# Kernel tuning notes

Measured on AMD Instinct MI355X. Metric: run time of the kernel, lower is better.

The kernel has to match this reference:

```python
import jax, jax.numpy as jnp
import numpy as np

N = 50000      # nodes
E = 600000     # edges
DIN = 128      # dim_in
DOUT = 128     # dim_out (mulhead=1)
DG = 64        # dim_gate


def setup_inputs() -> dict:
    key = jax.random.key(0)
    ks = jax.random.split(key, 10)
    rows = jax.random.randint(ks[0], (E,), 0, N, dtype=jnp.int32)   # dest nodes
    cols = jax.random.randint(ks[1], (E,), 0, N, dtype=jnp.int32)   # src nodes
    vals = jax.random.uniform(ks[2], (E,), dtype=jnp.float32)       # adj_norm values
    feat = jax.random.normal(ks[3], (N, DIN), dtype=jnp.float32)
    s = 1.0 / np.sqrt(DIN)
    W0 = jax.random.normal(ks[4], (DIN, DOUT), dtype=jnp.float32) * s
    b0 = jnp.zeros((DOUT,), dtype=jnp.float32)
    W1 = jax.random.normal(ks[5], (DIN, DOUT), dtype=jnp.float32) * s
    b1 = jnp.zeros((DOUT,), dtype=jnp.float32)
    att = jax.random.normal(ks[6], (2 * DOUT,), dtype=jnp.float32) * 0.1  # attention param [1, 2*DOUT] flattened
    W_pool = jax.random.normal(ks[7], (DIN, DG), dtype=jnp.float32) * s    # weight_pool_gate
    W_gate = jax.random.normal(ks[8], (2 * DIN + DG, 1), dtype=jnp.float32) * 0.05  # weight_gate, mulhead=1
    offset0 = jnp.zeros((DOUT,), dtype=jnp.float32)
    scale0 = jnp.ones((DOUT,), dtype=jnp.float32)
    offset1 = jnp.zeros((DOUT,), dtype=jnp.float32)
    scale1 = jnp.ones((DOUT,), dtype=jnp.float32)
    return dict(rows=rows, cols=cols, vals=vals, feat=feat, W0=W0, b0=b0,
                W1=W1, b1=b1, att=att, W_pool=W_pool, W_gate=W_gate,
                offset0=offset0, scale0=scale0, offset1=offset1, scale1=scale1)


def _batch_norm(x, scale, offset):
    # per-node norm over the feature dim (unbiased=False), matching _batch_norm
    m = x.mean(axis=1, keepdims=True)
    v = x.var(axis=1, keepdims=True) + 1e-9
    return (x - m) * scale * jax.lax.rsqrt(v) + offset


def reference(rows, cols, vals, feat, W0, b0, W1, b1, att, W_pool, W_gate,
              offset0, scale0, offset1, scale1):
    n = feat.shape[0]
    d = W0.shape[1]
    # --- gate value (GaAN eq. 3) ---
    zj = feat @ W_pool                                   # [N, DG]
    neigh_zj = jax.ops.segment_max(zj[cols], rows, num_segments=n)  # per-row max over neighbors
    neigh_zj = jnp.where(jnp.isfinite(neigh_zj), neigh_zj, 0.0)     # empty rows -> zeros
    neigh_mean = jax.ops.segment_sum(vals[:, None] * feat[cols], rows, num_segments=n)  # spmm(adj, feat)
    gate = jnp.concatenate([feat, neigh_zj, neigh_mean], axis=1) @ W_gate  # [N, 1]
    # --- per-order feature transforms (order=1, mulhead=1) ---
    h0 = jax.nn.relu(feat @ W0 + b0)                     # order 0 (self)
    h1 = jax.nn.relu(feat @ W1 + b1)                     # order 1 (neighbor)
    # --- sparse attention aggregation ---
    a_self = jax.nn.leaky_relu(h0 @ att[:d], 0.2)        # [N]
    a_neigh = jax.nn.leaky_relu(h1 @ att[d:], 0.2)       # [N]
    e = a_self[rows] + a_neigh[cols]                     # per-edge score (replaces adj values)
    agg = jax.ops.segment_sum(e[:, None] * h1[cols], rows, num_segments=n)  # spmm(att_adj, h1)
    agg = agg * gate[:, :1]                              # gated
    # --- per-node batch norm, then 'mean' aggregation (sum of orders) ---
    return _batch_norm(h0, scale0, offset0) + _batch_norm(agg, scale1, offset1)
```

## Files before the change

kernel.cpp:

```cpp
#include <hip/hip_runtime.h>

#define DIN 128
#define DG 64

typedef __attribute__((ext_vector_type(8))) short short8;
typedef __attribute__((ext_vector_type(4))) float f32x4;

static __device__ __forceinline__ unsigned short f2bf(float x) {
    unsigned u = __builtin_bit_cast(unsigned, x);
    u = (u + 0x7FFF + ((u >> 16) & 1)) >> 16;
    return (unsigned short)u;
}
static __device__ __forceinline__ float bf2f(unsigned short s) {
    return __builtin_bit_cast(float, (unsigned)s << 16);
}
static __device__ __forceinline__ float bflo(unsigned u) {
    return __builtin_bit_cast(float, u << 16);
}
static __device__ __forceinline__ float bfhi(unsigned u) {
    return __builtin_bit_cast(float, u & 0xFFFF0000u);
}


__global__ void k_pre(const int* __restrict__ rows, int* __restrict__ deg,
                      int* __restrict__ slot, int E, int nDeg,
                      const float* __restrict__ W0, const float* __restrict__ W1,
                      unsigned short* __restrict__ Bt) {
    int b = blockIdx.x;
    if (b < nDeg) {
        int e = b * 256 + threadIdx.x;
        if (e < E) slot[e] = atomicAdd(&deg[rows[e]], 1);
    } else {
        int k = b - nDeg;
        int c = threadIdx.x;
        const float* W = (c < 128) ? W0 : W1;
        Bt[c * 128 + k] = f2bf(W[k * 128 + (c & 127)]);
    }
}

#define AS_LD 132
#define ALD 136
#define SMEM_BYTES 25088

static __device__ __forceinline__ void zj_body(
    const float* __restrict__ feat, const float* __restrict__ Wp,
    const float* __restrict__ Wg,
    char* __restrict__ pack, float* __restrict__ gpart, float* __restrict__ fdotg,
    int N, char* smem) {
    float* As = (float*)smem;
    float* Bs = (float*)(smem + 32 * AS_LD * 4);
    int tid = threadIdx.x;
    int tx = tid & 15, ty = tid >> 4;
    int m0 = blockIdx.x * 128;
    if (m0 >= N) return;
    float acc[8][4];
    #pragma unroll
    for (int r = 0; r < 8; ++r)
        #pragma unroll
        for (int c = 0; c < 4; ++c) acc[r][c] = 0.f;
    float gdot[8], fdot[8];
    #pragma unroll
    for (int r = 0; r < 8; ++r) { gdot[r] = 0.f; fdot[r] = 0.f; }
    for (int kc = 0; kc < 128; kc += 32) {
        for (int i = tid; i < 1024; i += 256) {
            int m = i >> 3, kq = (i & 7) << 2;
            int node = m0 + m;
            float4 f;
            if (node < N) f = *(const float4*)&feat[(size_t)node * 128 + kc + kq];
            else          f = make_float4(0.f, 0.f, 0.f, 0.f);
            As[(kq + 0) * AS_LD + m] = f.x;
            As[(kq + 1) * AS_LD + m] = f.y;
            As[(kq + 2) * AS_LD + m] = f.z;
            As[(kq + 3) * AS_LD + m] = f.w;
        }
        for (int i = tid; i < 512; i += 256) {
            int k = i >> 4, cq = (i & 15) << 2;
            *(float4*)&Bs[k * 64 + cq] = *(const float4*)&Wp[(size_t)(kc + k) * 64 + cq];
        }
        __syncthreads();
        #pragma unroll 8
        for (int kk = 0; kk < 32; ++kk) {
            const float* ar = &As[kk * AS_LD];
            float4 a0 = *(const float4*)(ar + 4 * tx);
            float4 a1 = *(const float4*)(ar + 64 + 4 * tx);
            float4 b0v = *(const float4*)&Bs[kk * 64 + 4 * ty];
            float a[8] = {a0.x, a0.y, a0.z, a0.w, a1.x, a1.y, a1.z, a1.w};
            #pragma unroll
            for (int r = 0; r < 8; ++r) {
                acc[r][0] += a[r] * b0v.x; acc[r][1] += a[r] * b0v.y;
                acc[r][2] += a[r] * b0v.z; acc[r][3] += a[r] * b0v.w;
            }
            float g1 = Wg[kc + kk];
            float g2 = Wg[192 + kc + kk];
            #pragma unroll
            for (int r = 0; r < 8; ++r) { gdot[r] += a[r] * g1; fdot[r] += a[r] * g2; }
        }
        __syncthreads();
    }
    #pragma unroll
    for (int r = 0; r < 8; ++r) {
        int node = m0 + ((r < 4) ? (4 * tx + r) : (64 + 4 * tx + (r - 4)));
        if (node >= N) continue;
        char* rb = pack + (size_t)node * 512 + (size_t)ty * 32 + 8;
        *(float2*)(rb)      = make_float2(acc[r][0], acc[r][1]);
        *(float2*)(rb + 16) = make_float2(acc[r][2], acc[r][3]);
        if (ty == 0) { gpart[node] = gdot[r]; fdotg[node] = fdot[r]; }
    }
}

static __device__ __forceinline__ void mfma_body(
    const float* __restrict__ feat, const unsigned short* __restrict__ Bt,
    const float* __restrict__ b0, const float* __restrict__ b1,
    const float* __restrict__ att,
    float* __restrict__ h0, char* __restrict__ pack,
    float* __restrict__ a_self, float* __restrict__ a_neigh, int N, char* smem) {
    unsigned short* As = (unsigned short*)smem;
    float* sredA = (float*)(smem + 64 * ALD * 2);
    float* nredA = sredA + 128;
    int tid = threadIdx.x;
    int m0 = blockIdx.x * 64;
    for (int i = tid; i < 2048; i += 256) {
        int row = i >> 5, ch = i & 31;
        int node = m0 + row;
        float4 f;
        if (node < N) f = *(const float4*)&feat[(size_t)node * 128 + ch * 4];
        else          f = make_float4(0.f, 0.f, 0.f, 0.f);
        unsigned p0 = (unsigned)f2bf(f.x) | ((unsigned)f2bf(f.y) << 16);
        unsigned p1 = (unsigned)f2bf(f.z) | ((unsigned)f2bf(f.w) << 16);
        *(uint2*)&As[row * ALD + ch * 4] = make_uint2(p0, p1);
    }
    __syncthreads();
    int w = tid >> 6, lane = tid & 63;
    int lm = lane & 15, q = lane >> 4;
    f32x4 acc[4][4];
    #pragma unroll
    for (int rt = 0; rt < 4; ++rt)
        #pragma unroll
        for (int ct = 0; ct < 4; ++ct)
            #pragma unroll
            for (int r = 0; r < 4; ++r) acc[rt][ct][r] = 0.f;
    #pragma unroll
    for (int ks = 0; ks < 4; ++ks) {
        short8 a[4], b[4];
        #pragma unroll
        for (int rt = 0; rt < 4; ++rt)
            a[rt] = *(const short8*)&As[(rt * 16 + lm) * ALD + ks * 32 + q * 8];
        #pragma unroll
        for (int ct = 0; ct < 4; ++ct)
            b[ct] = *(const short8*)&Bt[(size_t)(w * 64 + ct * 16 + lm) * 128 + ks * 32 + q * 8];
        #pragma unroll
        for (int rt = 0; rt < 4; ++rt)
            #pragma unroll
            for (int ct = 0; ct < 4; ++ct)
                acc[rt][ct] = __builtin_amdgcn_mfma_f32_16x16x32_bf16(a[rt], b[ct], acc[rt][ct], 0, 0, 0);
    }
    float sacc[4][4];
    #pragma unroll
    for (int rt = 0; rt < 4; ++rt)
        #pragma unroll
        for (int r = 0; r < 4; ++r) sacc[rt][r] = 0.f;
    #pragma unroll
    for (int ct = 0; ct < 4; ++ct) {
        int col = w * 64 + ct * 16 + lm;
        float attc = att[col];
        float bias = (w < 2) ? b0[col] : b1[col - 128];
        int cp = col - 128;
        int pofs = ((cp >> 2) * 16 + (cp & 3) * 2);
        #pragma unroll
        for (int rt = 0; rt < 4; ++rt) {
            #pragma unroll
            for (int r = 0; r < 4; ++r) {
                float v = acc[rt][ct][r] + bias;
                v = fmaxf(v, 0.f);
                sacc[rt][r] += v * attc;
                int node = m0 + rt * 16 + q * 4 + r;
                if (node < N) {
                    if (w < 2) h0[(size_t)node * 128 + col] = v;
                    else       *(unsigned short*)(pack + (size_t)node * 512 + pofs) = f2bf(v);
                }
            }
        }
    }
    float* red = (w < 2) ? sredA : nredA;
    #pragma unroll
    for (int rt = 0; rt < 4; ++rt)
        #pragma unroll
        for (int r = 0; r < 4; ++r) {
            float s = sacc[rt][r];
            s += __shfl_xor(s, 1, 64); s += __shfl_xor(s, 2, 64);
            s += __shfl_xor(s, 4, 64); s += __shfl_xor(s, 8, 64);
            if (lm == 0) red[(w & 1) * 64 + rt * 16 + q * 4 + r] = s;
        }
    __syncthreads();
    if (tid < 64) {
        int node = m0 + tid;
        if (node < N) {
            float s  = sredA[tid] + sredA[64 + tid];
            float nn = nredA[tid] + nredA[64 + tid];
            a_self[node]  = (s  >= 0.f) ? s  : 0.2f * s;
            a_neigh[node] = (nn >= 0.f) ? nn : 0.2f * nn;
        }
    }
}

static __device__ __forceinline__ void scan_body(
    const int* __restrict__ deg, int* __restrict__ rowptr,
    unsigned long long* __restrict__ bstate, int n, int nbs, char* smem) {
    int b = blockIdx.x;
    if (b >= nbs) return;
    int* wsum = (int*)smem;
    int* bprefs = (int*)smem + 8;
    int tid = threadIdx.x, lane = tid & 63, w = tid >> 6;
    int base = b * 1024 + tid * 4;
    int4 v = make_int4(0, 0, 0, 0);
    if (base + 3 < n) v = *(const int4*)&deg[base];
    else {
        if (base     < n) v.x = deg[base];
        if (base + 1 < n) v.y = deg[base + 1];
        if (base + 2 < n) v.z = deg[base + 2];
        if (base + 3 < n) v.w = deg[base + 3];
    }
    int s = v.x + v.y + v.z + v.w;
    int x = s;
    #pragma unroll
    for (int off = 1; off < 64; off <<= 1) {
        int y = __shfl_up(x, off, 64);
        if (lane >= off) x += y;
    }
    if (lane == 63) wsum[w] = x;
    __syncthreads();
    int wpref = 0;
    for (int t = 0; t < w; ++t) wpref += wsum[t];
    int btotal = wsum[0] + wsum[1] + wsum[2] + wsum[3];
    int excl = x - s + wpref;
    if (tid == 0) {
        unsigned long long pack =
            ((unsigned long long)(b == 0 ? 2u : 1u) << 32) | (unsigned)btotal;
        atomicExch(&bstate[b], pack);
        int pref = 0;
        if (b > 0) {
            int i = b - 1;
            while (i >= 0) {
                unsigned long long st = atomicAdd(&bstate[i], 0ULL);
                unsigned f = (unsigned)(st >> 32);
                if (f == 0) { __builtin_amdgcn_s_sleep(1); continue; }
                pref += (int)(st & 0xffffffffULL);
                if (f == 2) break;
                --i;
            }
            atomicExch(&bstate[b], (2ULL << 32) | (unsigned)(pref + btotal));
        }
        bprefs[0] = pref;
    }
    __syncthreads();
    int p = bprefs[0] + excl;
    if (base + 3 < n) {
        *(int4*)&rowptr[base] = make_int4(p, p + v.x, p + v.x + v.y, p + v.x + v.y + v.z);
    } else {
        if (base     < n) rowptr[base]     = p;
        if (base + 1 < n) rowptr[base + 1] = p + v.x;
        if (base + 2 < n) rowptr[base + 2] = p + v.x + v.y;
        if (base + 3 < n) rowptr[base + 3] = p + v.x + v.y + v.z;
    }
    if (b == nbs - 1 && tid == 0) rowptr[n] = bprefs[0] + btotal;
}

__global__ __launch_bounds__(256) void k_fused(
    const float* __restrict__ feat, const float* __restrict__ Wp,
    const unsigned short* __restrict__ Bt,
    const float* __restrict__ b0, const float* __restrict__ b1,
    const float* __restrict__ att, const float* __restrict__ Wg,
    float* __restrict__ h0, char* __restrict__ pack,
    float* __restrict__ gpart, float* __restrict__ fdotg,
    float* __restrict__ a_self, float* __restrict__ a_neigh,
    const int* __restrict__ deg, int* __restrict__ rowptr,
    unsigned long long* __restrict__ bstate, int nbs, int N) {
    __shared__ __align__(16) char smem[SMEM_BYTES];
    if (blockIdx.y == 0)
        zj_body(feat, Wp, Wg, pack, gpart, fdotg, N, smem);
    else if (blockIdx.y == 1)
        mfma_body(feat, Bt, b0, b1, att, h0, pack, a_self, a_neigh, N, smem);
    else
        scan_body(deg, rowptr, bstate, N, nbs, smem);
}

__global__ void k_scatter_meta(const int* __restrict__ rows, const int* __restrict__ cols,
                               const float* __restrict__ vals,
                               const int* __restrict__ rowptr, const int* __restrict__ slot,
                               const float* __restrict__ a_neigh, const float* __restrict__ fdotg,
                               float4* __restrict__ meta, int E) {
    int e = blockIdx.x * blockDim.x + threadIdx.x;
    if (e < E) {
        int c = cols[e];
        int dst = rowptr[rows[e]] + slot[e];
        meta[dst] = make_float4(__builtin_bit_cast(float, c << 9),
                                a_neigh[c], vals[e] * fdotg[c], 0.f);
    }
}

__global__ __launch_bounds__(256) void k_aggregate(
    const float4* __restrict__ meta, const int* __restrict__ rowptr,
    const float* __restrict__ h0, const char* __restrict__ pack,
    const float* __restrict__ a_self, const float* __restrict__ gpart,
    const float* __restrict__ Wg,
    const float* __restrict__ scale0, const float* __restrict__ offset0,
    const float* __restrict__ scale1, const float* __restrict__ offset1,
    float* __restrict__ out, int N) {
    int wid = threadIdx.x >> 6;
    int lane = threadIdx.x & 63;
    int sub = lane >> 5;
    int l = lane & 31;
    int r = blockIdx.x * 8 + wid * 2 + sub;
    int rr = (r < N) ? r : (N - 1);
    int jb = rowptr[rr], je = rowptr[rr + 1];
    int trips = (je - jb + 7) >> 3;
    int tother = __shfl_xor(trips, 32, 64);
    int tmax = (trips > tother) ? trips : tother;
    int jclamp = (je > 0) ? je - 1 : 0;
    float asr = a_self[rr];
    const char* packl = pack + l * 16;
    float4 acc = make_float4(0.f, 0.f, 0.f, 0.f);
    float2 zmax = make_float2(-__builtin_inff(), -__builtin_inff());
    float vfsum = 0.f;
    for (int t0 = 0; t0 < tmax; ++t0) {
        int j = jb + t0 * 8;
        int joff[8]; float esv[8];
        #pragma unroll
        for (int t = 0; t < 8; ++t) {
            int jj = j + t;
            bool a = jj < je;
            float4 mt = meta[a ? jj : jclamp];
            joff[t] = __builtin_bit_cast(int, mt.x);
            esv[t] = a ? (asr + mt.y) : 0.f;
            vfsum += a ? mt.z : 0.f;
        }
        uint4 v[8];
        #pragma unroll
        for (int t = 0; t < 8; ++t)
            v[t] = *(const uint4*)(packl + (size_t)(unsigned)joff[t]);
        #pragma unroll
        for (int t = 0; t < 8; ++t) {
            float e = esv[t];
            acc.x += e * bflo(v[t].x);
            acc.y += e * bfhi(v[t].x);
            acc.z += e * bflo(v[t].y);
            acc.w += e * bfhi(v[t].y);
            zmax.x = fmaxf(zmax.x, __builtin_bit_cast(float, v[t].z));
            zmax.y = fmaxf(zmax.y, __builtin_bit_cast(float, v[t].w));
        }
    }
    if (jb == je) { zmax.x = 0.f; zmax.y = 0.f; }
    float gs = zmax.x * Wg[128 + 2 * l] + zmax.y * Wg[129 + 2 * l];
    #pragma unroll
    for (int off = 16; off; off >>= 1) gs += __shfl_xor(gs, off, 64);
    float gate = gpart[rr] + gs + vfsum;
    float4 ag = make_float4(acc.x * gate, acc.y * gate, acc.z * gate, acc.w * gate);
    float4 x0 = ((const float4*)(h0 + (size_t)rr * 128))[l];
    float m0s = x0.x + x0.y + x0.z + x0.w;
    #pragma unroll
    for (int off = 16; off; off >>= 1) m0s += __shfl_xor(m0s, off, 64);
    float m0 = m0s * (1.f / 128.f);
    float4 d0 = make_float4(x0.x - m0, x0.y - m0, x0.z - m0, x0.w - m0);
    float v0s = d0.x * d0.x + d0.y * d0.y + d0.z * d0.z + d0.w * d0.w;
    #pragma unroll
    for (int off = 16; off; off >>= 1) v0s += __shfl_xor(v0s, off, 64);
    float inv0 = rsqrtf(v0s * (1.f / 128.f) + 1e-9f);
    float m1s = ag.x + ag.y + ag.z + ag.w;
    #pragma unroll
    for (int off = 16; off; off >>= 1) m1s += __shfl_xor(m1s, off, 64);
    float m1 = m1s * (1.f / 128.f);
    float4 d1 = make_float4(ag.x - m1, ag.y - m1, ag.z - m1, ag.w - m1);
    float v1s = d1.x * d1.x + d1.y * d1.y + d1.z * d1.z + d1.w * d1.w;
    #pragma unroll
    for (int off = 16; off; off >>= 1) v1s += __shfl_xor(v1s, off, 64);
    float inv1 = rsqrtf(v1s * (1.f / 128.f) + 1e-9f);
    if (r >= N) return;
    float4 sc0 = ((const float4*)scale0)[l], of0 = ((const float4*)offset0)[l];
    float4 sc1 = ((const float4*)scale1)[l], of1 = ((const float4*)offset1)[l];
    float4 o;
    o.x = d0.x * sc0.x * inv0 + of0.x + d1.x * sc1.x * inv1 + of1.x;
    o.y = d0.y * sc0.y * inv0 + of0.y + d1.y * sc1.y * inv1 + of1.y;
    o.z = d0.z * sc0.z * inv0 + of0.z + d1.z * sc1.z * inv1 + of1.z;
    o.w = d0.w * sc0.w * inv0 + of0.w + d1.w * sc1.w * inv1 + of1.w;
    ((float4*)(out + (size_t)r * 128))[l] = o;
}

extern "C" void kernel_launch(void* const* d_in, const int* in_sizes, int n_in,
                              void* d_out, int out_size, void* d_ws, size_t ws_size,
                              hipStream_t stream) {
    const int*   rows   = (const int*)d_in[0];
    const int*   cols   = (const int*)d_in[1];
    const float* vals   = (const float*)d_in[2];
    const float* feat   = (const float*)d_in[3];
    const float* W0     = (const float*)d_in[4];
    const float* b0     = (const float*)d_in[5];
    const float* W1     = (const float*)d_in[6];
    const float* b1     = (const float*)d_in[7];
    const float* att    = (const float*)d_in[8];
    const float* Wp     = (const float*)d_in[9];
    const float* Wg     = (const float*)d_in[10];
    const float* offset0 = (const float*)d_in[11];
    const float* scale0  = (const float*)d_in[12];
    const float* offset1 = (const float*)d_in[13];
    const float* scale1  = (const float*)d_in[14];
    float* out = (float*)d_out;

    const int E = in_sizes[0];
    const int N = in_sizes[3] / DIN;
    const int Npad = (N + 63) & ~63;

    char* ws = (char*)d_ws;
    float* h0          = (float*)ws;          ws += (size_t)N * 128 * sizeof(float);
    char* pack         = ws;                  ws += (size_t)N * 512;
    unsigned short* Bt = (unsigned short*)ws; ws += (size_t)256 * 128 * sizeof(unsigned short);
    float* a_self  = (float*)ws; ws += (size_t)N * sizeof(float);
    float* a_neigh = (float*)ws; ws += (size_t)N * sizeof(float);
    float* gpart   = (float*)ws; ws += (size_t)N * sizeof(float);
    float* fdotg   = (float*)ws; ws += (size_t)N * sizeof(float);
    ws = (char*)(((size_t)ws + 7) & ~(size_t)7);
    unsigned long long* bstate = (unsigned long long*)ws; ws += 64 * sizeof(unsigned long long);
    int* deg      = (int*)ws; ws += (size_t)(N + 1) * sizeof(int);
    int* rowptr   = (int*)ws; ws += (size_t)(N + 1) * sizeof(int);
    int* slot     = (int*)ws; ws += (size_t)E * sizeof(int);
    ws = (char*)(((size_t)ws + 15) & ~(size_t)15);
    float4* meta  = (float4*)ws; ws += (size_t)E * sizeof(float4);

    hipMemsetAsync(bstate, 0, 64 * sizeof(unsigned long long) + (size_t)(N + 1) * sizeof(int), stream);

    int nDeg = (E + 255) / 256;
    k_pre<<<nDeg + 128, 256, 0, stream>>>(rows, deg, slot, E, nDeg, W0, W1, Bt);

    int nbs = (N + 1023) >> 10;
    dim3 gg(Npad / 64, 3);
    k_fused<<<gg, 256, 0, stream>>>(feat, Wp, Bt, b0, b1, att, Wg,
                                    h0, pack, gpart, fdotg, a_self, a_neigh,
                                    deg, rowptr, bstate, nbs, N);

    k_scatter_meta<<<nDeg, 256, 0, stream>>>(rows, cols, vals, rowptr, slot,
                                             a_neigh, fdotg, meta, E);

    int nb8 = (N + 7) / 8;
    k_aggregate<<<nb8, 256, 0, stream>>>(meta, rowptr, h0, pack,
                                         a_self, gpart, Wg,
                                         scale0, offset0, scale1, offset1, out, N);
}
```

Measured before the change: 250.2 us.

## Fuse pooling GEMM and gate dots into MFMA block, stage pack rows in LDS

```diff
diff --git a/kernel.cpp b/kernel.cpp
--- a/kernel.cpp
+++ b/kernel.cpp
@@ -38,85 +38,23 @@
     }
 }
 
-#define AS_LD 132
 #define ALD 136
-#define SMEM_BYTES 25088
-
-static __device__ __forceinline__ void zj_body(
-    const float* __restrict__ feat, const float* __restrict__ Wp,
-    const float* __restrict__ Wg,
-    char* __restrict__ pack, float* __restrict__ gpart, float* __restrict__ fdotg,
-    int N, char* smem) {
-    float* As = (float*)smem;
-    float* Bs = (float*)(smem + 32 * AS_LD * 4);
-    int tid = threadIdx.x;
-    int tx = tid & 15, ty = tid >> 4;
-    int m0 = blockIdx.x * 128;
-    if (m0 >= N) return;
-    float acc[8][4];
-    #pragma unroll
-    for (int r = 0; r < 8; ++r)
-        #pragma unroll
-        for (int c = 0; c < 4; ++c) acc[r][c] = 0.f;
-    float gdot[8], fdot[8];
-    #pragma unroll
-    for (int r = 0; r < 8; ++r) { gdot[r] = 0.f; fdot[r] = 0.f; }
-    for (int kc = 0; kc < 128; kc += 32) {
-        for (int i = tid; i < 1024; i += 256) {
-            int m = i >> 3, kq = (i & 7) << 2;
-            int node = m0 + m;
-            float4 f;
-            if (node < N) f = *(const float4*)&feat[(size_t)node * 128 + kc + kq];
-            else          f = make_float4(0.f, 0.f, 0.f, 0.f);
-            As[(kq + 0) * AS_LD + m] = f.x;
-            As[(kq + 1) * AS_LD + m] = f.y;
-            As[(kq + 2) * AS_LD + m] = f.z;
-            As[(kq + 3) * AS_LD + m] = f.w;
-        }
-        for (int i = tid; i < 512; i += 256) {
-            int k = i >> 4, cq = (i & 15) << 2;
-            *(float4*)&Bs[k * 64 + cq] = *(const float4*)&Wp[(size_t)(kc + k) * 64 + cq];
-        }
-        __syncthreads();
-        #pragma unroll 8
-        for (int kk = 0; kk < 32; ++kk) {
-            const float* ar = &As[kk * AS_LD];
-            float4 a0 = *(const float4*)(ar + 4 * tx);
-            float4 a1 = *(const float4*)(ar + 64 + 4 * tx);
-            float4 b0v = *(const float4*)&Bs[kk * 64 + 4 * ty];
-            float a[8] = {a0.x, a0.y, a0.z, a0.w, a1.x, a1.y, a1.z, a1.w};
-            #pragma unroll
-            for (int r = 0; r < 8; ++r) {
-                acc[r][0] += a[r] * b0v.x; acc[r][1] += a[r] * b0v.y;
-                acc[r][2] += a[r] * b0v.z; acc[r][3] += a[r] * b0v.w;
-            }
-            float g1 = Wg[kc + kk];
-            float g2 = Wg[192 + kc + kk];
-            #pragma unroll
-            for (int r = 0; r < 8; ++r) { gdot[r] += a[r] * g1; fdot[r] += a[r] * g2; }
-        }
-        __syncthreads();
-    }
-    #pragma unroll
-    for (int r = 0; r < 8; ++r) {
-        int node = m0 + ((r < 4) ? (4 * tx + r) : (64 + 4 * tx + (r - 4)));
-        if (node >= N) continue;
-        char* rb = pack + (size_t)node * 512 + (size_t)ty * 32 + 8;
-        *(float2*)(rb)      = make_float2(acc[r][0], acc[r][1]);
-        *(float2*)(rb + 16) = make_float2(acc[r][2], acc[r][3]);
-        if (ty == 0) { gpart[node] = gdot[r]; fdotg[node] = fdot[r]; }
-    }
-}
+#define AFLD 132
+#define SMEM_BYTES 52224
 
 static __device__ __forceinline__ void mfma_body(
     const float* __restrict__ feat, const unsigned short* __restrict__ Bt,
     const float* __restrict__ b0, const float* __restrict__ b1,
-    const float* __restrict__ att,
+    const float* __restrict__ att, const float* __restrict__ Wp,
+    const float* __restrict__ Wg,
     float* __restrict__ h0, char* __restrict__ pack,
-    float* __restrict__ a_self, float* __restrict__ a_neigh, int N, char* smem) {
-    unsigned short* As = (unsigned short*)smem;
-    float* sredA = (float*)(smem + 64 * ALD * 2);
+    float* __restrict__ gpart, float* __restrict__ anf,
+    float* __restrict__ a_self, int N, char* smem) {
+    unsigned short* Ah = (unsigned short*)smem;
+    float* Af = (float*)(smem + 17408);
+    float* sredA = (float*)(smem + 51200);
     float* nredA = sredA + 128;
+    char* pb = smem + 17408;
     int tid = threadIdx.x;
     int m0 = blockIdx.x * 64;
     for (int i = tid; i < 2048; i += 256) {
@@ -125,13 +63,58 @@
         float4 f;
         if (node < N) f = *(const float4*)&feat[(size_t)node * 128 + ch * 4];
         else          f = make_float4(0.f, 0.f, 0.f, 0.f);
+        *(float4*)&Af[row * AFLD + ch * 4] = f;
         unsigned p0 = (unsigned)f2bf(f.x) | ((unsigned)f2bf(f.y) << 16);
         unsigned p1 = (unsigned)f2bf(f.z) | ((unsigned)f2bf(f.w) << 16);
-        *(uint2*)&As[row * ALD + ch * 4] = make_uint2(p0, p1);
+        *(uint2*)&Ah[row * ALD + ch * 4] = make_uint2(p0, p1);
     }
     __syncthreads();
     int w = tid >> 6, lane = tid & 63;
     int lm = lane & 15, q = lane >> 4;
+
+    int c4 = lane & 15;
+    int r4 = lane >> 4;
+    float zacc[4][4];
+    #pragma unroll
+    for (int a = 0; a < 4; ++a)
+        #pragma unroll
+        for (int c = 0; c < 4; ++c) zacc[a][c] = 0.f;
+    {
+        const float* afr = &Af[(w * 16 + r4 * 4) * AFLD];
+        #pragma unroll 2
+        for (int k = 0; k < 128; k += 4) {
+            float4 w0 = *(const float4*)&Wp[(k + 0) * 64 + c4 * 4];
+            float4 w1 = *(const float4*)&Wp[(k + 1) * 64 + c4 * 4];
+            float4 w2 = *(const float4*)&Wp[(k + 2) * 64 + c4 * 4];
+            float4 w3 = *(const float4*)&Wp[(k + 3) * 64 + c4 * 4];
+            #pragma unroll
+            for (int rr = 0; rr < 4; ++rr) {
+                float4 fv = *(const float4*)&afr[rr * AFLD + k];
+                zacc[rr][0] += fv.x * w0.x + fv.y * w1.x + fv.z * w2.x + fv.w * w3.x;
+                zacc[rr][1] += fv.x * w0.y + fv.y * w1.y + fv.z * w2.y + fv.w * w3.y;
+                zacc[rr][2] += fv.x * w0.z + fv.y * w1.z + fv.z * w2.z + fv.w * w3.z;
+                zacc[rr][3] += fv.x * w0.w + fv.y * w1.w + fv.z * w2.w + fv.w * w3.w;
+            }
+        }
+    }
+    float gdot;
+    {
+        int grow = lane >> 2;
+        int pairsel = (lane >> 1) & 1;
+        int half = lane & 1;
+        const float* wg = Wg + pairsel * 192 + half * 64;
+        const float* af2 = &Af[(w * 16 + grow) * AFLD + half * 64];
+        float d = 0.f;
+        #pragma unroll 4
+        for (int k = 0; k < 64; k += 4) {
+            float4 f = *(const float4*)&af2[k];
+            float4 g = *(const float4*)&wg[k];
+            d += f.x * g.x + f.y * g.y + f.z * g.z + f.w * g.w;
+        }
+        d += __shfl_xor(d, 1, 64);
+        gdot = d;
+    }
+
     f32x4 acc[4][4];
     #pragma unroll
     for (int rt = 0; rt < 4; ++rt)
@@ -144,7 +127,7 @@
         short8 a[4], b[4];
         #pragma unroll
         for (int rt = 0; rt < 4; ++rt)
-            a[rt] = *(const short8*)&As[(rt * 16 + lm) * ALD + ks * 32 + q * 8];
+            a[rt] = *(const short8*)&Ah[(rt * 16 + lm) * ALD + ks * 32 + q * 8];
         #pragma unroll
         for (int ct = 0; ct < 4; ++ct)
             b[ct] = *(const short8*)&Bt[(size_t)(w * 64 + ct * 16 + lm) * 128 + ks * 32 + q * 8];
@@ -154,6 +137,8 @@
             for (int ct = 0; ct < 4; ++ct)
                 acc[rt][ct] = __builtin_amdgcn_mfma_f32_16x16x32_bf16(a[rt], b[ct], acc[rt][ct], 0, 0, 0);
     }
+    __syncthreads();
+
     float sacc[4][4];
     #pragma unroll
     for (int rt = 0; rt < 4; ++rt)
@@ -165,7 +150,7 @@
         float attc = att[col];
         float bias = (w < 2) ? b0[col] : b1[col - 128];
         int cp = col - 128;
-        int pofs = ((cp >> 2) * 16 + (cp & 3) * 2);
+        int pofs = (cp >> 2) * 16 + (cp & 3) * 2;
         #pragma unroll
         for (int rt = 0; rt < 4; ++rt) {
             #pragma unroll
@@ -173,12 +158,29 @@
                 float v = acc[rt][ct][r] + bias;
                 v = fmaxf(v, 0.f);
                 sacc[rt][r] += v * attc;
-                int node = m0 + rt * 16 + q * 4 + r;
-                if (node < N) {
-                    if (w < 2) h0[(size_t)node * 128 + col] = v;
-                    else       *(unsigned short*)(pack + (size_t)node * 512 + pofs) = f2bf(v);
+                int row = rt * 16 + q * 4 + r;
+                if (w < 2) {
+                    int node = m0 + row;
+                    if (node < N) h0[(size_t)node * 128 + col] = v;
+                } else {
+                    *(unsigned short*)(pb + row * 512 + pofs) = f2bf(v);
                 }
             }
+        }
+    }
+    #pragma unroll
+    for (int rr = 0; rr < 4; ++rr) {
+        int row = w * 16 + r4 * 4 + rr;
+        char* prow = pb + row * 512 + 8 + c4 * 32;
+        *(float2*)(prow)      = make_float2(zacc[rr][0], zacc[rr][1]);
+        *(float2*)(prow + 16) = make_float2(zacc[rr][2], zacc[rr][3]);
+    }
+    {
+        int grow = lane >> 2;
+        int node = m0 + w * 16 + grow;
+        if (node < N) {
+            if ((lane & 3) == 0)      gpart[node] = gdot;
+            else if ((lane & 3) == 2) anf[2 * (size_t)node + 1] = gdot;
         }
     }
     float* red = (w < 2) ? sredA : nredA;
@@ -192,13 +194,17 @@
             if (lm == 0) red[(w & 1) * 64 + rt * 16 + q * 4 + r] = s;
         }
     __syncthreads();
+    for (int i = tid; i < 2048; i += 256) {
+        float4 val = *(const float4*)(pb + i * 16);
+        *(float4*)(pack + (size_t)(m0 + (i >> 5)) * 512 + (i & 31) * 16) = val;
+    }
     if (tid < 64) {
         int node = m0 + tid;
         if (node < N) {
             float s  = sredA[tid] + sredA[64 + tid];
             float nn = nredA[tid] + nredA[64 + tid];
-            a_self[node]  = (s  >= 0.f) ? s  : 0.2f * s;
-            a_neigh[node] = (nn >= 0.f) ? nn : 0.2f * nn;
+            a_self[node] = (s  >= 0.f) ? s  : 0.2f * s;
+            anf[2 * (size_t)node] = (nn >= 0.f) ? nn : 0.2f * nn;
         }
     }
 }
@@ -234,9 +240,9 @@
     int btotal = wsum[0] + wsum[1] + wsum[2] + wsum[3];
     int excl = x - s + wpref;
     if (tid == 0) {
-        unsigned long long pack =
+        unsigned long long pk =
             ((unsigned long long)(b == 0 ? 2u : 1u) << 32) | (unsigned)btotal;
-        atomicExch(&bstate[b], pack);
+        atomicExch(&bstate[b], pk);
         int pref = 0;
         if (b > 0) {
             int i = b - 1;
@@ -266,20 +272,18 @@
 }
 
 __global__ __launch_bounds__(256) void k_fused(
-    const float* __restrict__ feat, const float* __restrict__ Wp,
-    const unsigned short* __restrict__ Bt,
+    const float* __restrict__ feat, const unsigned short* __restrict__ Bt,
     const float* __restrict__ b0, const float* __restrict__ b1,
-    const float* __restrict__ att, const float* __restrict__ Wg,
+    const float* __restrict__ att, const float* __restrict__ Wp,
+    const float* __restrict__ Wg,
     float* __restrict__ h0, char* __restrict__ pack,
-    float* __restrict__ gpart, float* __restrict__ fdotg,
-    float* __restrict__ a_self, float* __restrict__ a_neigh,
+    float* __restrict__ gpart, float* __restrict__ anf,
+    float* __restrict__ a_self,
     const int* __restrict__ deg, int* __restrict__ rowptr,
     unsigned long long* __restrict__ bstate, int nbs, int N) {
     __shared__ __align__(16) char smem[SMEM_BYTES];
     if (blockIdx.y == 0)
-        zj_body(feat, Wp, Wg, pack, gpart, fdotg, N, smem);
-    else if (blockIdx.y == 1)
-        mfma_body(feat, Bt, b0, b1, att, h0, pack, a_self, a_neigh, N, smem);
+        mfma_body(feat, Bt, b0, b1, att, Wp, Wg, h0, pack, gpart, anf, a_self, N, smem);
     else
         scan_body(deg, rowptr, bstate, N, nbs, smem);
 }
@@ -287,14 +291,15 @@
 __global__ void k_scatter_meta(const int* __restrict__ rows, const int* __restrict__ cols,
                                const float* __restrict__ vals,
                                const int* __restrict__ rowptr, const int* __restrict__ slot,
-                               const float* __restrict__ a_neigh, const float* __restrict__ fdotg,
+                               const float* __restrict__ anf,
                                float4* __restrict__ meta, int E) {
     int e = blockIdx.x * blockDim.x + threadIdx.x;
     if (e < E) {
         int c = cols[e];
         int dst = rowptr[rows[e]] + slot[e];
+        float2 av = *(const float2*)&anf[2 * (size_t)c];
         meta[dst] = make_float4(__builtin_bit_cast(float, c << 9),
-                                a_neigh[c], vals[e] * fdotg[c], 0.f);
+                                av.x, vals[e] * av.y, 0.f);
     }
 }
 
@@ -411,12 +416,11 @@
 
     char* ws = (char*)d_ws;
     float* h0          = (float*)ws;          ws += (size_t)N * 128 * sizeof(float);
-    char* pack         = ws;                  ws += (size_t)N * 512;
+    char* pack         = ws;                  ws += (size_t)Npad * 512;
     unsigned short* Bt = (unsigned short*)ws; ws += (size_t)256 * 128 * sizeof(unsigned short);
     float* a_self  = (float*)ws; ws += (size_t)N * sizeof(float);
-    float* a_neigh = (float*)ws; ws += (size_t)N * sizeof(float);
+    float* anf     = (float*)ws; ws += (size_t)N * 2 * sizeof(float);
     float* gpart   = (float*)ws; ws += (size_t)N * sizeof(float);
-    float* fdotg   = (float*)ws; ws += (size_t)N * sizeof(float);
     ws = (char*)(((size_t)ws + 7) & ~(size_t)7);
     unsigned long long* bstate = (unsigned long long*)ws; ws += 64 * sizeof(unsigned long long);
     int* deg      = (int*)ws; ws += (size_t)(N + 1) * sizeof(int);
@@ -431,13 +435,13 @@
     k_pre<<<nDeg + 128, 256, 0, stream>>>(rows, deg, slot, E, nDeg, W0, W1, Bt);
 
     int nbs = (N + 1023) >> 10;
-    dim3 gg(Npad / 64, 3);
-    k_fused<<<gg, 256, 0, stream>>>(feat, Wp, Bt, b0, b1, att, Wg,
-                                    h0, pack, gpart, fdotg, a_self, a_neigh,
+    dim3 gg(Npad / 64, 2);
+    k_fused<<<gg, 256, 0, stream>>>(feat, Bt, b0, b1, att, Wp, Wg,
+                                    h0, pack, gpart, anf, a_self,
                                     deg, rowptr, bstate, nbs, N);
 
     k_scatter_meta<<<nDeg, 256, 0, stream>>>(rows, cols, vals, rowptr, slot,
-                                             a_neigh, fdotg, meta, E);
+                                             anf, meta, E);
 
     int nb8 = (N + 7) / 8;
     k_aggregate<<<nb8, 256, 0, stream>>>(meta, rowptr, h0, pack,
```

After: 252.7 us. About the same (+1.0%).

## Move zj GEMM into pre kernel and stage pack rows in LDS for coalesced stores

Applied to the files above, without the earlier changes.

```diff
diff --git a/kernel.cpp b/kernel.cpp
--- a/kernel.cpp
+++ b/kernel.cpp
@@ -22,36 +22,19 @@
 }
 
 
-__global__ void k_pre(const int* __restrict__ rows, int* __restrict__ deg,
-                      int* __restrict__ slot, int E, int nDeg,
-                      const float* __restrict__ W0, const float* __restrict__ W1,
-                      unsigned short* __restrict__ Bt) {
-    int b = blockIdx.x;
-    if (b < nDeg) {
-        int e = b * 256 + threadIdx.x;
-        if (e < E) slot[e] = atomicAdd(&deg[rows[e]], 1);
-    } else {
-        int k = b - nDeg;
-        int c = threadIdx.x;
-        const float* W = (c < 128) ? W0 : W1;
-        Bt[c * 128 + k] = f2bf(W[k * 128 + (c & 127)]);
-    }
-}
-
 #define AS_LD 132
-#define ALD 136
-#define SMEM_BYTES 25088
+#define ZJ_SMEM 25088
 
 static __device__ __forceinline__ void zj_body(
     const float* __restrict__ feat, const float* __restrict__ Wp,
     const float* __restrict__ Wg,
-    char* __restrict__ pack, float* __restrict__ gpart, float* __restrict__ fdotg,
-    int N, char* smem) {
+    float* __restrict__ zjc, float* __restrict__ gpart, float* __restrict__ anf,
+    int zb, int N, char* smem) {
     float* As = (float*)smem;
     float* Bs = (float*)(smem + 32 * AS_LD * 4);
     int tid = threadIdx.x;
     int tx = tid & 15, ty = tid >> 4;
-    int m0 = blockIdx.x * 128;
+    int m0 = zb * 128;
     if (m0 >= N) return;
     float acc[8][4];
     #pragma unroll
@@ -101,22 +84,51 @@
     for (int r = 0; r < 8; ++r) {
         int node = m0 + ((r < 4) ? (4 * tx + r) : (64 + 4 * tx + (r - 4)));
         if (node >= N) continue;
-        char* rb = pack + (size_t)node * 512 + (size_t)ty * 32 + 8;
-        *(float2*)(rb)      = make_float2(acc[r][0], acc[r][1]);
-        *(float2*)(rb + 16) = make_float2(acc[r][2], acc[r][3]);
-        if (ty == 0) { gpart[node] = gdot[r]; fdotg[node] = fdot[r]; }
-    }
-}
+        *(float4*)&zjc[(size_t)node * 64 + 4 * ty] =
+            make_float4(acc[r][0], acc[r][1], acc[r][2], acc[r][3]);
+        if (ty == 0) { gpart[node] = gdot[r]; anf[2 * (size_t)node + 1] = fdot[r]; }
+    }
+}
+
+__global__ void k_pre(const int* __restrict__ rows, int* __restrict__ deg,
+                      int* __restrict__ slot, int E, int nDeg,
+                      const float* __restrict__ W0, const float* __restrict__ W1,
+                      unsigned short* __restrict__ Bt,
+                      const float* __restrict__ feat, const float* __restrict__ Wp,
+                      const float* __restrict__ Wg,
+                      float* __restrict__ zjc, float* __restrict__ gpart,
+                      float* __restrict__ anf, int N) {
+    __shared__ __align__(16) char smem[ZJ_SMEM];
+    int b = blockIdx.x;
+    if (b < nDeg) {
+        int e = b * 256 + threadIdx.x;
+        if (e < E) slot[e] = atomicAdd(&deg[rows[e]], 1);
+        return;
+    }
+    if (b < nDeg + 128) {
+        int k = b - nDeg;
+        int c = threadIdx.x;
+        const float* W = (c < 128) ? W0 : W1;
+        Bt[c * 128 + k] = f2bf(W[k * 128 + (c & 127)]);
+        return;
+    }
+    zj_body(feat, Wp, Wg, zjc, gpart, anf, b - nDeg - 128, N, smem);
+}
+
+#define ALD 136
+#define RED_OFF 32768
+#define SMEM_BYTES 33792
 
 static __device__ __forceinline__ void mfma_body(
     const float* __restrict__ feat, const unsigned short* __restrict__ Bt,
     const float* __restrict__ b0, const float* __restrict__ b1,
-    const float* __restrict__ att,
+    const float* __restrict__ att, const float* __restrict__ zjc,
     float* __restrict__ h0, char* __restrict__ pack,
-    float* __restrict__ a_self, float* __restrict__ a_neigh, int N, char* smem) {
-    unsigned short* As = (unsigned short*)smem;
-    float* sredA = (float*)(smem + 64 * ALD * 2);
+    float* __restrict__ anf, float* __restrict__ a_self, int N, char* smem) {
+    unsigned short* Ah = (unsigned short*)smem;
+    float* sredA = (float*)(smem + RED_OFF);
     float* nredA = sredA + 128;
+    char* pb = smem;
     int tid = threadIdx.x;
     int m0 = blockIdx.x * 64;
     for (int i = tid; i < 2048; i += 256) {
@@ -127,7 +139,7 @@
         else          f = make_float4(0.f, 0.f, 0.f, 0.f);
         unsigned p0 = (unsigned)f2bf(f.x) | ((unsigned)f2bf(f.y) << 16);
         unsigned p1 = (unsigned)f2bf(f.z) | ((unsigned)f2bf(f.w) << 16);
-        *(uint2*)&As[row * ALD + ch * 4] = make_uint2(p0, p1);
+        *(uint2*)&Ah[row * ALD + ch * 4] = make_uint2(p0, p1);
     }
     __syncthreads();
     int w = tid >> 6, lane = tid & 63;
@@ -144,7 +156,7 @@
         short8 a[4], b[4];
         #pragma unroll
         for (int rt = 0; rt < 4; ++rt)
-            a[rt] = *(const short8*)&As[(rt * 16 + lm) * ALD + ks * 32 + q * 8];
+            a[rt] = *(const short8*)&Ah[(rt * 16 + lm) * ALD + ks * 32 + q * 8];
         #pragma unroll
         for (int ct = 0; ct < 4; ++ct)
             b[ct] = *(const short8*)&Bt[(size_t)(w * 64 + ct * 16 + lm) * 128 + ks * 32 + q * 8];
@@ -154,6 +166,8 @@
             for (int ct = 0; ct < 4; ++ct)
                 acc[rt][ct] = __builtin_amdgcn_mfma_f32_16x16x32_bf16(a[rt], b[ct], acc[rt][ct], 0, 0, 0);
     }
+    __syncthreads();
+
     float sacc[4][4];
     #pragma unroll
     for (int rt = 0; rt < 4; ++rt)
@@ -165,7 +179,7 @@
         float attc = att[col];
         float bias = (w < 2) ? b0[col] : b1[col - 128];
         int cp = col - 128;
-        int pofs = ((cp >> 2) * 16 + (cp & 3) * 2);
+        int pofs = (cp >> 2) * 16 + (cp & 3) * 2;
         #pragma unroll
         for (int rt = 0; rt < 4; ++rt) {
             #pragma unroll
@@ -173,13 +187,25 @@
                 float v = acc[rt][ct][r] + bias;
                 v = fmaxf(v, 0.f);
                 sacc[rt][r] += v * attc;
-                int node = m0 + rt * 16 + q * 4 + r;
-                if (node < N) {
-                    if (w < 2) h0[(size_t)node * 128 + col] = v;
-                    else       *(unsigned short*)(pack + (size_t)node * 512 + pofs) = f2bf(v);
+                int row = rt * 16 + q * 4 + r;
+                if (w < 2) {
+                    int node = m0 + row;
+                    if (node < N) h0[(size_t)node * 128 + col] = v;
+                } else {
+                    *(unsigned short*)(pb + row * 512 + pofs) = f2bf(v);
                 }
             }
         }
+    }
+    for (int i = tid; i < 1024; i += 256) {
+        int row = i >> 4, cq = i & 15;
+        int node = m0 + row;
+        float4 z;
+        if (node < N) z = *(const float4*)&zjc[(size_t)node * 64 + cq * 4];
+        else          z = make_float4(0.f, 0.f, 0.f, 0.f);
+        char* prow = pb + row * 512 + cq * 32 + 8;
+        *(float2*)(prow)      = make_float2(z.x, z.y);
+        *(float2*)(prow + 16) = make_float2(z.z, z.w);
     }
     float* red = (w < 2) ? sredA : nredA;
     #pragma unroll
@@ -192,13 +218,17 @@
             if (lm == 0) red[(w & 1) * 64 + rt * 16 + q * 4 + r] = s;
         }
     __syncthreads();
+    for (int i = tid; i < 2048; i += 256) {
+        float4 val = *(const float4*)(pb + i * 16);
+        *(float4*)(pack + (size_t)(m0 + (i >> 5)) * 512 + (i & 31) * 16) = val;
+    }
     if (tid < 64) {
         int node = m0 + tid;
         if (node < N) {
             float s  = sredA[tid] + sredA[64 + tid];
             float nn = nredA[tid] + nredA[64 + tid];
-            a_self[node]  = (s  >= 0.f) ? s  : 0.2f * s;
-            a_neigh[node] = (nn >= 0.f) ? nn : 0.2f * nn;
+            a_self[node] = (s  >= 0.f) ? s  : 0.2f * s;
+            anf[2 * (size_t)node] = (nn >= 0.f) ? nn : 0.2f * nn;
         }
     }
 }
@@ -234,9 +264,9 @@
     int btotal = wsum[0] + wsum[1] + wsum[2] + wsum[3];
     int excl = x - s + wpref;
     if (tid == 0) {
-        unsigned long long pack =
+        unsigned long long pk =
             ((unsigned long long)(b == 0 ? 2u : 1u) << 32) | (unsigned)btotal;
-        atomicExch(&bstate[b], pack);
+        atomicExch(&bstate[b], pk);
         int pref = 0;
         if (b > 0) {
             int i = b - 1;
@@ -266,20 +296,16 @@
 }
 
 __global__ __launch_bounds__(256) void k_fused(
-    const float* __restrict__ feat, const float* __restrict__ Wp,
-    const unsigned short* __restrict__ Bt,
+    const float* __restrict__ feat, const unsigned short* __restrict__ Bt,
     const float* __restrict__ b0, const float* __restrict__ b1,
-    const float* __restrict__ att, const float* __restrict__ Wg,
+    const float* __restrict__ att, const float* __restrict__ zjc,
     float* __restrict__ h0, char* __restrict__ pack,
-    float* __restrict__ gpart, float* __restrict__ fdotg,
-    float* __restrict__ a_self, float* __restrict__ a_neigh,
+    float* __restrict__ anf, float* __restrict__ a_self,
     const int* __restrict__ deg, int* __restrict__ rowptr,
     unsigned long long* __restrict__ bstate, int nbs, int N) {
     __shared__ __align__(16) char smem[SMEM_BYTES];
     if (blockIdx.y == 0)
-        zj_body(feat, Wp, Wg, pack, gpart, fdotg, N, smem);
-    else if (blockIdx.y == 1)
-        mfma_body(feat, Bt, b0, b1, att, h0, pack, a_self, a_neigh, N, smem);
+        mfma_body(feat, Bt, b0, b1, att, zjc, h0, pack, anf, a_self, N, smem);
     else
         scan_body(deg, rowptr, bstate, N, nbs, smem);
 }
@@ -287,14 +313,15 @@
 __global__ void k_scatter_meta(const int* __restrict__ rows, const int* __restrict__ cols,
                                const float* __restrict__ vals,
                                const int* __restrict__ rowptr, const int* __restrict__ slot,
-                               const float* __restrict__ a_neigh, const float* __restrict__ fdotg,
+                               const float* __restrict__ anf,
                                float4* __restrict__ meta, int E) {
     int e = blockIdx.x * blockDim.x + threadIdx.x;
     if (e < E) {
         int c = cols[e];
         int dst = rowptr[rows[e]] + slot[e];
+        float2 av = *(const float2*)&anf[2 * (size_t)c];
         meta[dst] = make_float4(__builtin_bit_cast(float, c << 9),
-                                a_neigh[c], vals[e] * fdotg[c], 0.f);
+                                av.x, vals[e] * av.y, 0.f);
     }
 }
 
@@ -411,12 +438,12 @@
 
     char* ws = (char*)d_ws;
     float* h0          = (float*)ws;          ws += (size_t)N * 128 * sizeof(float);
-    char* pack         = ws;                  ws += (size_t)N * 512;
+    char* pack         = ws;                  ws += (size_t)Npad * 512;
     unsigned short* Bt = (unsigned short*)ws; ws += (size_t)256 * 128 * sizeof(unsigned short);
     float* a_self  = (float*)ws; ws += (size_t)N * sizeof(float);
-    float* a_neigh = (float*)ws; ws += (size_t)N * sizeof(float);
+    float* anf     = (float*)ws; ws += (size_t)N * 2 * sizeof(float);
     float* gpart   = (float*)ws; ws += (size_t)N * sizeof(float);
-    float* fdotg   = (float*)ws; ws += (size_t)N * sizeof(float);
+    float* zjc     = (float*)ws; ws += (size_t)N * 64 * sizeof(float);
     ws = (char*)(((size_t)ws + 7) & ~(size_t)7);
     unsigned long long* bstate = (unsigned long long*)ws; ws += 64 * sizeof(unsigned long long);
     int* deg      = (int*)ws; ws += (size_t)(N + 1) * sizeof(int);
@@ -428,16 +455,18 @@
     hipMemsetAsync(bstate, 0, 64 * sizeof(unsigned long long) + (size_t)(N + 1) * sizeof(int), stream);
 
     int nDeg = (E + 255) / 256;
-    k_pre<<<nDeg + 128, 256, 0, stream>>>(rows, deg, slot, E, nDeg, W0, W1, Bt);
+    int nZj = (N + 127) / 128;
+    k_pre<<<nDeg + 128 + nZj, 256, 0, stream>>>(rows, deg, slot, E, nDeg, W0, W1, Bt,
+                                                feat, Wp, Wg, zjc, gpart, anf, N);
 
     int nbs = (N + 1023) >> 10;
-    dim3 gg(Npad / 64, 3);
-    k_fused<<<gg, 256, 0, stream>>>(feat, Wp, Bt, b0, b1, att, Wg,
-                                    h0, pack, gpart, fdotg, a_self, a_neigh,
+    dim3 gg(Npad / 64, 2);
+    k_fused<<<gg, 256, 0, stream>>>(feat, Bt, b0, b1, att, zjc,
+                                    h0, pack, anf, a_self,
                                     deg, rowptr, bstate, nbs, N);
 
     k_scatter_meta<<<nDeg, 256, 0, stream>>>(rows, cols, vals, rowptr, slot,
-                                             a_neigh, fdotg, meta, E);
+                                             anf, meta, E);
 
     int nb8 = (N + 7) / 8;
     k_aggregate<<<nb8, 256, 0, stream>>>(meta, rowptr, h0, pack,
```

After: 266.7 us. +6.6%, slower.
